# Optimization experiments

Measured on AMD Instinct MI355X. Metric: run time of the kernel, lower is better.

## Reference

```python
import jax, jax.numpy as jnp
import numpy as np
import math

DIM_IN, DIM_OUT, DIM_HID = 128, 128, 512
DEPTH, HEADS, DIM_HEAD, MLP = 6, 8, 64, 2048
INNER = HEADS * DIM_HEAD  # 512


def _inorm(t, eps=1e-5):
    # torch InstanceNorm1d on ((b h), n, d): normalize over last (spatial) dim, biased var, no affine
    m = jnp.mean(t, axis=-1, keepdims=True)
    v = jnp.mean((t - m) ** 2, axis=-1, keepdims=True)
    return (t - m) * jax.lax.rsqrt(v + eps)


def _layernorm(t, g, b, eps=1e-5):
    m = jnp.mean(t, axis=-1, keepdims=True)
    v = jnp.mean((t - m) ** 2, axis=-1, keepdims=True)
    return (t - m) * jax.lax.rsqrt(v + eps) * g + b


def _pos_encoding(n, d):
    pos = jnp.arange(n, dtype=jnp.float32)[:, None]
    div = jnp.exp(jnp.arange(0, d, 2, dtype=jnp.float32) * (-math.log(10000.0) / d))
    pe = jnp.zeros((n, d), dtype=jnp.float32)
    pe = pe.at[:, 0::2].set(jnp.sin(pos * div))
    pe = pe.at[:, 1::2].set(jnp.cos(pos * div))
    return pe


def setup_inputs() -> dict:
    key = jax.random.key(0)
    ks = jax.random.split(key, 16)
    s = 0.02
    return {
        "x": jax.random.normal(ks[0], (4, 64, 4096, 2), jnp.float32),
        "W_emb": jax.random.normal(ks[1], (DIM_IN, DIM_HID), jnp.float32) * s,
        "b_emb": jnp.zeros((DIM_HID,), jnp.float32),
        "ln_g": jnp.ones((DEPTH, DIM_HID), jnp.float32),
        "ln_b": jnp.zeros((DEPTH, DIM_HID), jnp.float32),
        "Wqkv": jax.random.normal(ks[2], (DEPTH, DIM_HID, 3 * INNER), jnp.float32) * s,
        "Wout": jax.random.normal(ks[3], (DEPTH, INNER, DIM_HID), jnp.float32) * s,
        "b_out": jnp.zeros((DEPTH, DIM_HID), jnp.float32),
        "W1": jax.random.normal(ks[4], (DEPTH, DIM_HID, 2 * MLP), jnp.float32) * s,
        "b1": jnp.zeros((DEPTH, 2 * MLP), jnp.float32),
        "W2": jax.random.normal(ks[5], (DEPTH, MLP, DIM_HID), jnp.float32) * s,
        "b2": jnp.zeros((DEPTH, DIM_HID), jnp.float32),
        "Wd": jax.random.normal(ks[6], (DIM_HID, DIM_OUT), jnp.float32) * s,
        "bd": jnp.zeros((DIM_OUT,), jnp.float32),
    }


def reference(x, W_emb, b_emb, ln_g, ln_b, Wqkv, Wout, b_out, W1, b1, W2, b2, Wd, bd):
    b, t, n, c = x.shape
    h = x.transpose(0, 2, 1, 3).reshape(b, n, t * c)        # [b, n, dim_in]
    h = (h @ W_emb + b_emb) * math.sqrt(DIM_HID)
    h = h + _pos_encoding(n, DIM_HID)[None]                 # positional encoding (dropout=0)
    inv_n = 1.0 / n
    for i in range(DEPTH):
        # PreNorm(LinearAttention) + residual
        y = _layernorm(h, ln_g[i], ln_b[i])
        qkv = y @ Wqkv[i]                                   # [b, n, 3*inner]
        q, k, v = jnp.split(qkv, 3, axis=-1)
        sp = lambda z: z.reshape(b, n, HEADS, DIM_HEAD).transpose(0, 2, 1, 3)  # b h n d
        q, k, v = sp(q), sp(k), sp(v)
        k, v = _inorm(k), _inorm(v)                         # galerkin: norm K and V
        dots = jnp.einsum('bhnd,bhne->bhde', k, v)          # k^T v: O(n) attention
        o = jnp.einsum('bhnd,bhde->bhne', q, dots) * inv_n
        o = o.transpose(0, 2, 1, 3).reshape(b, n, INNER)
        h = o @ Wout[i] + b_out[i] + h
        # FeedForward (no PreNorm in galerkin branch) + residual
        f = h @ W1[i] + b1[i]
        f = jax.nn.gelu(f[..., :MLP], approximate=False) * f[..., MLP:]
        h = f @ W2[i] + b2[i] + h
    out = h @ Wd + bd                                       # [b, n, dim_out]
    return out.transpose(0, 2, 1).reshape(b, -1, 1)         # [b, dim_out*n, 1]
```

## Files before the change

### kernel.cpp

```cpp
#include <hip/hip_runtime.h>
#include <hip/hip_bf16.h>
#include <stdint.h>
#include <math.h>


typedef _Float16 f16x8 __attribute__((ext_vector_type(8)));
typedef float f32x4 __attribute__((ext_vector_type(4)));
typedef unsigned short u16x8 __attribute__((ext_vector_type(8)));
typedef unsigned short u16;

#define SEQ 4096
#define NTOK 16384
#define HID 512
#define RSCL 256.0f
#define RSCLI (1.0f/256.0f)

__device__ __forceinline__ float wred(float x) {
#pragma unroll
  for (int off = 32; off; off >>= 1) x += __shfl_xor(x, off);
  return x;
}

__device__ __forceinline__ u16 f2h(float v) {
  _Float16 h = (_Float16)v;
  return __builtin_bit_cast(u16, h);
}
__device__ __forceinline__ float h2f(u16 u) {
  return (float)__builtin_bit_cast(_Float16, u);
}

__device__ __forceinline__ float fgelu(float a) {
  float t = 0.7978845608f * a * (1.0f + 0.044715f * a * a);
  float e = __expf(2.0f * t);
  float th = 1.0f - 2.0f / (e + 1.0f);
  return 0.5f * a * (1.0f + th);
}

__device__ __forceinline__ void gload16(const void* g, void* l) {
  __builtin_amdgcn_global_load_lds(
      reinterpret_cast<const __attribute__((address_space(1))) int*>(
          reinterpret_cast<uintptr_t>(g)),
      reinterpret_cast<__attribute__((address_space(3))) int*>(
          reinterpret_cast<uintptr_t>(l)),
      16, 0, 0);
}

__device__ __forceinline__ void stS(const u16* g, int ldk, int rowBase, int k0,
                                    short* lds, int c) {
  int pr = c >> 3, s8 = (c & 7) ^ (pr & 7);
  int r = pr * 2 + (s8 >> 2);
  gload16(g + (size_t)(rowBase + r) * ldk + k0 + (s8 & 3) * 8, lds + c * 8);
}
__device__ __forceinline__ int idxg(int row, int grp) {
  int pr = row >> 1;
  int s8 = ((((row & 1) << 2) | grp) ^ (pr & 7));
  return pr * 64 + s8 * 8;
}

__global__ __launch_bounds__(256) void k_transpose(const float* __restrict__ src,
                                                   u16* __restrict__ dst,
                                                   int K, int N) {
  int d = blockIdx.z;
  const float* s = src + (size_t)d * K * N;
  u16* o = dst + (size_t)d * N * K;
  int k0 = blockIdx.x * 64, n0 = blockIdx.y * 64;
  __shared__ float tile[64][65];
  int t = threadIdx.x, c = t & 63, r4 = t >> 6;
#pragma unroll
  for (int i = 0; i < 16; ++i) {
    int r = i * 4 + r4;
    tile[r][c] = s[(size_t)(k0 + r) * N + n0 + c];
  }
  __syncthreads();
#pragma unroll
  for (int i = 0; i < 16; ++i) {
    int r = i * 4 + r4;
    o[(size_t)(n0 + r) * K + k0 + c] = f2h(tile[c][r]);
  }
}

__global__ __launch_bounds__(256) void k_packx(const float* __restrict__ x,
                                               u16* __restrict__ XP) {
  int idx = blockIdx.x * 256 + threadIdx.x;
  int k = idx & 127, row = idx >> 7;
  int b = row >> 12, n = row & 4095;
  int tt = k >> 1, c = k & 1;
  XP[idx] = f2h(x[(((size_t)(b * 64 + tt)) * SEQ + n) * 2 + c]);
}

__global__ __launch_bounds__(256) void k_ln(const float* __restrict__ H,
                                            const float* __restrict__ G,
                                            const float* __restrict__ B,
                                            u16* __restrict__ Y) {
  int t = threadIdx.x, lane = t & 63;
  int row = blockIdx.x * 4 + (t >> 6);
  const float4* h4 = (const float4*)(H + (size_t)row * HID);
  float4 a = h4[lane * 2], b = h4[lane * 2 + 1];
  float v[8] = {a.x, a.y, a.z, a.w, b.x, b.y, b.z, b.w};
  float s = v[0] + v[1] + v[2] + v[3] + v[4] + v[5] + v[6] + v[7];
  s = wred(s);
  float m = s * (1.0f / 512.0f);
  float q = 0.f;
#pragma unroll
  for (int i = 0; i < 8; ++i) {
    v[i] -= m;
    q += v[i] * v[i];
  }
  q = wred(q);
  float rs = rsqrtf(q * (1.0f / 512.0f) + 1e-5f);
  const float4* g4 = (const float4*)G;
  const float4* b4 = (const float4*)B;
  float4 g1 = g4[lane * 2], g2 = g4[lane * 2 + 1];
  float4 e1 = b4[lane * 2], e2 = b4[lane * 2 + 1];
  float gg[8] = {g1.x, g1.y, g1.z, g1.w, g2.x, g2.y, g2.z, g2.w};
  float ee[8] = {e1.x, e1.y, e1.z, e1.w, e2.x, e2.y, e2.z, e2.w};
  union { u16x8 v; u16 s_[8]; } uh;
#pragma unroll
  for (int i = 0; i < 8; ++i) uh.s_[i] = f2h(v[i] * rs * gg[i] + ee[i]);
  *reinterpret_cast<u16x8*>((u16*)Y + (size_t)row * HID + lane * 8) = uh.v;
}

__global__ __launch_bounds__(256) void k_dots(const u16* __restrict__ QKV,
                                              float* __restrict__ DOTSP) {
  int bh = blockIdx.y, b = bh >> 3, h = bh & 7;
  int n0 = blockIdx.x * 512;
  __shared__ alignas(16) short ks[64 * 64];
  __shared__ alignas(16) short vs[64 * 64];
  int t = threadIdx.x;
  int d0 = (t & 15) * 4, e0 = (t >> 4) * 4;
  float acc[4][4] = {};
  for (int sub = 0; sub < 8; ++sub) {
    int nb = n0 + sub * 64;
#pragma unroll
    for (int i = 0; i < 2; ++i) {
      int c = t + i * 256;
      int r = c >> 3, off = (c & 7) << 3;
      const u16* base = QKV + (size_t)(b * SEQ + nb + r) * 1536;
      gload16(base + 512 + h * 64 + off, ks + c * 8);
      gload16(base + 1024 + h * 64 + off, vs + c * 8);
    }
    asm volatile("s_waitcnt vmcnt(0)" ::: "memory");
    __syncthreads();
    for (int r = 0; r < 64; ++r) {
      short4 kk = *(const short4*)&ks[r * 64 + d0];
      short4 vv = *(const short4*)&vs[r * 64 + e0];
      float kf[4] = {h2f((u16)kk.x), h2f((u16)kk.y), h2f((u16)kk.z), h2f((u16)kk.w)};
      float vf[4] = {h2f((u16)vv.x), h2f((u16)vv.y), h2f((u16)vv.z), h2f((u16)vv.w)};
#pragma unroll
      for (int i = 0; i < 4; ++i)
#pragma unroll
        for (int j = 0; j < 4; ++j) acc[i][j] += kf[i] * vf[j];
    }
    __syncthreads();
  }
  float* dst = DOTSP + ((size_t)blockIdx.x * 32 + bh) * 4096;
#pragma unroll
  for (int i = 0; i < 4; ++i)
#pragma unroll
    for (int j = 0; j < 4; ++j) dst[(d0 + i) * 64 + e0 + j] = acc[i][j];
}

__global__ __launch_bounds__(256) void k_reddots(const float* __restrict__ P,
                                                 float* __restrict__ D) {
  int i = blockIdx.x * 256 + threadIdx.x;
  float s = 0.f;
#pragma unroll
  for (int c = 0; c < 8; ++c) s += P[(size_t)c * 131072 + i];
  D[i] = s;
}

__global__ __launch_bounds__(256) void k_ov(const u16* __restrict__ QKV,
                                            const float* __restrict__ DOTS,
                                            u16* __restrict__ O) {
  int bh = blockIdx.y, b = bh >> 3, h = bh & 7;
  int n0 = blockIdx.x * 64;
  __shared__ alignas(16) float ds[64 * 64];
  __shared__ alignas(16) short qs[64 * 64];
  int t = threadIdx.x;
  const float* dsrc = DOTS + (size_t)bh * 4096;
#pragma unroll
  for (int i = 0; i < 16; ++i) ds[t + i * 256] = dsrc[t + i * 256];
#pragma unroll
  for (int i = 0; i < 2; ++i) {
    int c = t + i * 256, r = c >> 3, off = (c & 7) << 3;
    gload16(QKV + (size_t)(b * SEQ + n0 + r) * 1536 + h * 64 + off, qs + c * 8);
  }
  asm volatile("s_waitcnt vmcnt(0)" ::: "memory");
  __syncthreads();
  int wv = t >> 6, lane = t & 63;
  for (int tok = wv; tok < 64; tok += 4) {
    float acc = 0.f;
#pragma unroll
    for (int d = 0; d < 64; d += 4) {
      short4 q4 = *(const short4*)&qs[tok * 64 + d];
      acc += h2f((u16)q4.x) * ds[(d + 0) * 64 + lane];
      acc += h2f((u16)q4.y) * ds[(d + 1) * 64 + lane];
      acc += h2f((u16)q4.z) * ds[(d + 2) * 64 + lane];
      acc += h2f((u16)q4.w) * ds[(d + 3) * 64 + lane];
    }
    O[(size_t)(b * SEQ + n0 + tok) * 512 + h * 64 + lane] = f2h(acc * (1.0f / SEQ));
  }
}

template <int MODE>
__global__ __launch_bounds__(256, 2) void k_gemm(
    const u16* __restrict__ A, const u16* __restrict__ B1, int K,
    const float* __restrict__ bias, const float* __restrict__ Hin,
    float ascale, float* __restrict__ out32, u16* __restrict__ o16, int ldo) {
  __shared__ alignas(16) short sm[2][2][4096];
  const int t = threadIdx.x, lane = t & 63;
  const int wv = t >> 6, wr = wv >> 1, wc = wv & 1;
  const int r16 = lane & 15, grp = lane >> 4;
  const int mBase = blockIdx.y * 128, nBase = blockIdx.x * 128;
  const int NT = K >> 5;

  f32x4 acc[4][4] = {};

  auto stage_all = [&](int sb, int k0) {
    stS(A, K, mBase, k0, &sm[sb][0][0], t);
    stS(A, K, mBase, k0, &sm[sb][0][0], t + 256);
    stS(B1, K, nBase, k0, &sm[sb][1][0], t);
    stS(B1, K, nBase, k0, &sm[sb][1][0], t + 256);
  };

  stage_all(0, 0);
  stage_all(1, 32);

  for (int kt = 0; kt < NT; ++kt) {
    const int cur = kt & 1;
    if (kt + 1 < NT) asm volatile("s_waitcnt vmcnt(4)" ::: "memory");
    else             asm volatile("s_waitcnt vmcnt(0)" ::: "memory");
    __builtin_amdgcn_s_barrier();
    f16x8 af[4], bv[4];
#pragma unroll
    for (int f = 0; f < 4; ++f)
      af[f] = *(const f16x8*)&sm[cur][0][idxg(wr * 64 + f * 16 + r16, grp)];
#pragma unroll
    for (int f = 0; f < 4; ++f)
      bv[f] = *(const f16x8*)&sm[cur][1][idxg(wc * 64 + f * 16 + r16, grp)];
    asm volatile("s_waitcnt lgkmcnt(0)" ::: "memory");
    __builtin_amdgcn_sched_barrier(0);
    __builtin_amdgcn_s_barrier();
    if (kt + 2 < NT) stage_all(cur, (kt + 2) << 5);
    __builtin_amdgcn_s_setprio(1);
#pragma unroll
    for (int i = 0; i < 4; ++i)
#pragma unroll
      for (int j = 0; j < 4; ++j)
        acc[i][j] = __builtin_amdgcn_mfma_f32_16x16x32_f16(af[i], bv[j], acc[i][j], 0, 0, 0);
    __builtin_amdgcn_s_setprio(0);
  }

  if constexpr (MODE == 1) {
    const bool doNorm = (nBase >= 512);
#pragma unroll
    for (int i = 0; i < 4; ++i) {
#pragma unroll
      for (int r = 0; r < 4; ++r) {
        float s = 0.f, s2 = 0.f;
#pragma unroll
        for (int j = 0; j < 4; ++j) {
          float v = acc[i][j][r];
          s += v;
          s2 += v * v;
        }
#pragma unroll
        for (int off = 8; off; off >>= 1) {
          s += __shfl_xor(s, off);
          s2 += __shfl_xor(s2, off);
        }
        float m = s * (1.0f / 64.0f);
        float var = fmaxf(s2 * (1.0f / 64.0f) - m * m, 0.f);
        float rs = rsqrtf(var + 1e-5f);
        int row = mBase + wr * 64 + i * 16 + grp * 4 + r;
#pragma unroll
        for (int j = 0; j < 4; ++j) {
          int col = nBase + wc * 64 + j * 16 + r16;
          float v = acc[i][j][r];
          if (doNorm) v = (v - m) * rs;
          o16[(size_t)row * ldo + col] = f2h(v);
        }
      }
    }
    return;
  }

#pragma unroll
  for (int i = 0; i < 4; ++i) {
#pragma unroll
    for (int j = 0; j < 4; ++j) {
#pragma unroll
      for (int r = 0; r < 4; ++r) {
        int row = mBase + wr * 64 + i * 16 + grp * 4 + r;
        int col = nBase + wc * 64 + j * 16 + r16;
        float v = acc[i][j][r];
        if constexpr (MODE == 0) {
          v = (v + bias[col]) * 22.627416997969522f;
          int n = row & (SEQ - 1);
          int k2 = col >> 1;
          float ang = (float)n * expf((float)k2 * -0.03597789207803197f);
          v += (col & 1) ? cosf(ang) : sinf(ang);
          out32[(size_t)row * HID + col] = v;
        } else if constexpr (MODE == 2) {
          v = v * ascale + bias[col] + Hin[(size_t)row * HID + col];
          out32[(size_t)row * HID + col] = v;
          o16[(size_t)row * HID + col] = f2h(v * RSCLI);
        } else {
          v = v * RSCL + bias[col];
          out32[(size_t)(row >> 12) * (128 * 4096) + (size_t)col * SEQ + (row & 4095)] = v;
        }
      }
    }
  }
}

__global__ __launch_bounds__(512, 2) void k_gemmG(
    const u16* __restrict__ A, int lda,
    const u16* __restrict__ B1, const u16* __restrict__ B2, int K,
    const float* __restrict__ bias, u16* __restrict__ o16, int ldo) {
  __shared__ alignas(16) short sm[2][20480];
  const int t = threadIdx.x, lane = t & 63;
  const int w = t >> 6, wr = w >> 2, wcn = w & 3;
  const int r16 = lane & 15, grp = lane >> 4;
  const int mBase = blockIdx.y * 128, nBase = blockIdx.x * 256;
  const int NT = K >> 5;

  f32x4 acc[4][4] = {};
  f32x4 acc2[4][4] = {};

  auto stage_all = [&](int sb, int k0) {
    stS(A, lda, mBase, k0, &sm[sb][0], t);
    stS(B1, K, nBase, k0, &sm[sb][4096], t);
    stS(B1, K, nBase, k0, &sm[sb][4096], t + 512);
    stS(B2, K, nBase, k0, &sm[sb][12288], t);
    stS(B2, K, nBase, k0, &sm[sb][12288], t + 512);
  };

  stage_all(0, 0);
  stage_all(1, 32);

  for (int kt = 0; kt < NT; ++kt) {
    const int cur = kt & 1;
    if (kt + 1 < NT) asm volatile("s_waitcnt vmcnt(5)" ::: "memory");
    else             asm volatile("s_waitcnt vmcnt(0)" ::: "memory");
    __builtin_amdgcn_s_barrier();
    f16x8 af[4], b1v[4], b2v[4];
#pragma unroll
    for (int i = 0; i < 4; ++i)
      af[i] = *(const f16x8*)&sm[cur][idxg(wr * 64 + i * 16 + r16, grp)];
#pragma unroll
    for (int j = 0; j < 4; ++j) {
      int ro = idxg(wcn * 64 + j * 16 + r16, grp);
      b1v[j] = *(const f16x8*)&sm[cur][4096 + ro];
      b2v[j] = *(const f16x8*)&sm[cur][12288 + ro];
    }
    asm volatile("s_waitcnt lgkmcnt(0)" ::: "memory");
    __builtin_amdgcn_sched_barrier(0);
    __builtin_amdgcn_s_barrier();
    if (kt + 2 < NT) stage_all(cur, (kt + 2) << 5);
    __builtin_amdgcn_s_setprio(1);
#pragma unroll
    for (int i = 0; i < 4; ++i)
#pragma unroll
      for (int j = 0; j < 4; ++j) {
        acc[i][j] = __builtin_amdgcn_mfma_f32_16x16x32_f16(af[i], b1v[j], acc[i][j], 0, 0, 0);
        acc2[i][j] = __builtin_amdgcn_mfma_f32_16x16x32_f16(af[i], b2v[j], acc2[i][j], 0, 0, 0);
      }
    __builtin_amdgcn_s_setprio(0);
  }

#pragma unroll
  for (int i = 0; i < 4; ++i) {
#pragma unroll
    for (int j = 0; j < 4; ++j) {
#pragma unroll
      for (int r = 0; r < 4; ++r) {
        int row = mBase + wr * 64 + i * 16 + grp * 4 + r;
        int col = nBase + wcn * 64 + j * 16 + r16;
        float a = acc[i][j][r] * RSCL + bias[col];
        float c2 = acc2[i][j][r] * RSCL + bias[2048 + col];
        o16[(size_t)row * ldo + col] = f2h(fgelu(a) * c2 * RSCLI);
      }
    }
  }
}

extern "C" void kernel_launch(void* const* d_in, const int* in_sizes, int n_in,
                              void* d_out, int out_size, void* d_ws, size_t ws_size,
                              hipStream_t stream) {
  const float* x    = (const float*)d_in[0];
  const float* Wemb = (const float*)d_in[1];
  const float* bemb = (const float*)d_in[2];
  const float* lng  = (const float*)d_in[3];
  const float* lnb  = (const float*)d_in[4];
  const float* Wqkv = (const float*)d_in[5];
  const float* Wout = (const float*)d_in[6];
  const float* bout = (const float*)d_in[7];
  const float* W1   = (const float*)d_in[8];
  const float* b1   = (const float*)d_in[9];
  const float* W2   = (const float*)d_in[10];
  const float* b2   = (const float*)d_in[11];
  const float* Wd   = (const float*)d_in[12];
  const float* bd   = (const float*)d_in[13];

  char* p = (char*)d_ws;
  auto alloc = [&](size_t bytes) {
    char* r = p;
    p += (bytes + 255) & ~(size_t)255;
    return r;
  };
  u16* WembT = (u16*)alloc((size_t)512 * 128 * 2);
  u16* WqkvT = (u16*)alloc((size_t)6 * 1536 * 512 * 2);
  u16* WoutT = (u16*)alloc((size_t)6 * 512 * 512 * 2);
  u16* W1T   = (u16*)alloc((size_t)6 * 4096 * 512 * 2);
  u16* W2T   = (u16*)alloc((size_t)6 * 512 * 2048 * 2);
  u16* WdT   = (u16*)alloc((size_t)128 * 512 * 2);
  float* H   = (float*)alloc((size_t)NTOK * 512 * 4);
  u16* HB    = (u16*)alloc((size_t)NTOK * 512 * 2);
  float* DOTSP = (float*)alloc((size_t)8 * 32 * 4096 * 4);
  float* DOTS  = (float*)alloc((size_t)32 * 4096 * 4);
  char* U = alloc((size_t)64 * 1024 * 1024);
  const size_t MI = 1024 * 1024;
  u16* XP  = (u16*)U;
  u16* Y   = (u16*)U;
  u16* QKV = (u16*)(U + 16 * MI);
  u16* O   = (u16*)U;
  u16* F   = (u16*)U;

  k_transpose<<<dim3(2, 8, 1),  256, 0, stream>>>(Wemb, WembT, 128, 512);
  k_transpose<<<dim3(8, 24, 6), 256, 0, stream>>>(Wqkv, WqkvT, 512, 1536);
  k_transpose<<<dim3(8, 8, 6),  256, 0, stream>>>(Wout, WoutT, 512, 512);
  k_transpose<<<dim3(8, 64, 6), 256, 0, stream>>>(W1, W1T, 512, 4096);
  k_transpose<<<dim3(32, 8, 6), 256, 0, stream>>>(W2, W2T, 2048, 512);
  k_transpose<<<dim3(8, 2, 1),  256, 0, stream>>>(Wd, WdT, 512, 128);

  k_packx<<<8192, 256, 0, stream>>>(x, XP);
  k_gemm<0><<<dim3(4, 128), 256, 0, stream>>>(XP, WembT, 128, bemb,
      nullptr, 1.f, H, nullptr, 0);

  for (int i = 0; i < 6; ++i) {
    k_ln<<<4096, 256, 0, stream>>>(H, lng + i * 512, lnb + i * 512, Y);
    k_gemm<1><<<dim3(12, 128), 256, 0, stream>>>(Y,
        WqkvT + (size_t)i * 1536 * 512, 512, nullptr, nullptr, 1.f,
        nullptr, QKV, 1536);
    k_dots<<<dim3(8, 32), 256, 0, stream>>>(QKV, DOTSP);
    k_reddots<<<512, 256, 0, stream>>>(DOTSP, DOTS);
    k_ov<<<dim3(64, 32), 256, 0, stream>>>(QKV, DOTS, O);
    k_gemm<2><<<dim3(4, 128), 256, 0, stream>>>(O,
        WoutT + (size_t)i * 512 * 512, 512, bout + i * 512, H, 1.f, H, HB, 512);
    k_gemmG<<<dim3(8, 128), 512, 0, stream>>>(HB, 512,
        W1T + (size_t)i * 4096 * 512,
        W1T + (size_t)i * 4096 * 512 + (size_t)2048 * 512, 512,
        b1 + i * 4096, F, 2048);
    k_gemm<2><<<dim3(4, 128), 256, 0, stream>>>(F,
        W2T + (size_t)i * 512 * 2048, 2048, b2 + i * 512, H, RSCL, H, HB, 512);
  }
  k_gemm<7><<<dim3(1, 128), 256, 0, stream>>>(HB, WdT, 512, bd,
      nullptr, 1.f, (float*)d_out, nullptr, 0);
}
```

Measured before the change: 1.815 ms.

## Stage K/V/Q as fp32 in LDS, register-tile o=q·dots, move GEMM restaging after MFMAs

k_dots and k_ov now load fp16 QKV through registers, convert to fp32 once and store fp32 tiles in LDS, so the inner loops no longer convert halves repeatedly. k_ov switches from one token per wave with scalar LDS reads to a 4x4 register tile per thread with float4 loads and vectorized stores. Both GEMM kernels move the barrier and next-stage global-to-LDS load to after the MFMA block, so fragment reads no longer wait on an extra barrier. The cost is double the LDS footprint for the staging tiles and less overlap between the next tile's loads and the MFMAs.

```diff
diff --git a/kernel.cpp b/kernel.cpp
--- a/kernel.cpp
+++ b/kernel.cpp
@@ -124,34 +124,47 @@
                                               float* __restrict__ DOTSP) {
   int bh = blockIdx.y, b = bh >> 3, h = bh & 7;
   int n0 = blockIdx.x * 512;
-  __shared__ alignas(16) short ks[64 * 64];
-  __shared__ alignas(16) short vs[64 * 64];
+  __shared__ alignas(16) float ksf[64 * 64];
+  __shared__ alignas(16) float vsf[64 * 64];
   int t = threadIdx.x;
   int d0 = (t & 15) * 4, e0 = (t >> 4) * 4;
   float acc[4][4] = {};
   for (int sub = 0; sub < 8; ++sub) {
     int nb = n0 + sub * 64;
+    u16x8 kreg[2], vreg[2];
+    int rr[2], oo[2];
 #pragma unroll
     for (int i = 0; i < 2; ++i) {
       int c = t + i * 256;
-      int r = c >> 3, off = (c & 7) << 3;
-      const u16* base = QKV + (size_t)(b * SEQ + nb + r) * 1536;
-      gload16(base + 512 + h * 64 + off, ks + c * 8);
-      gload16(base + 1024 + h * 64 + off, vs + c * 8);
-    }
-    asm volatile("s_waitcnt vmcnt(0)" ::: "memory");
+      rr[i] = c >> 3;
+      oo[i] = (c & 7) << 3;
+      const u16* base = QKV + (size_t)(b * SEQ + nb + rr[i]) * 1536 + h * 64 + oo[i];
+      kreg[i] = *(const u16x8*)(base + 512);
+      vreg[i] = *(const u16x8*)(base + 1024);
+    }
+    __syncthreads();
+#pragma unroll
+    for (int i = 0; i < 2; ++i) {
+      float4 k0 = {h2f(kreg[i][0]), h2f(kreg[i][1]), h2f(kreg[i][2]), h2f(kreg[i][3])};
+      float4 k1 = {h2f(kreg[i][4]), h2f(kreg[i][5]), h2f(kreg[i][6]), h2f(kreg[i][7])};
+      float4 v0 = {h2f(vreg[i][0]), h2f(vreg[i][1]), h2f(vreg[i][2]), h2f(vreg[i][3])};
+      float4 v1 = {h2f(vreg[i][4]), h2f(vreg[i][5]), h2f(vreg[i][6]), h2f(vreg[i][7])};
+      *(float4*)&ksf[rr[i] * 64 + oo[i]] = k0;
+      *(float4*)&ksf[rr[i] * 64 + oo[i] + 4] = k1;
+      *(float4*)&vsf[rr[i] * 64 + oo[i]] = v0;
+      *(float4*)&vsf[rr[i] * 64 + oo[i] + 4] = v1;
+    }
     __syncthreads();
     for (int r = 0; r < 64; ++r) {
-      short4 kk = *(const short4*)&ks[r * 64 + d0];
-      short4 vv = *(const short4*)&vs[r * 64 + e0];
-      float kf[4] = {h2f((u16)kk.x), h2f((u16)kk.y), h2f((u16)kk.z), h2f((u16)kk.w)};
-      float vf[4] = {h2f((u16)vv.x), h2f((u16)vv.y), h2f((u16)vv.z), h2f((u16)vv.w)};
+      float4 kk = *(const float4*)&ksf[r * 64 + d0];
+      float4 vv = *(const float4*)&vsf[r * 64 + e0];
+      float kf[4] = {kk.x, kk.y, kk.z, kk.w};
+      float vf[4] = {vv.x, vv.y, vv.z, vv.w};
 #pragma unroll
       for (int i = 0; i < 4; ++i)
 #pragma unroll
         for (int j = 0; j < 4; ++j) acc[i][j] += kf[i] * vf[j];
     }
-    __syncthreads();
   }
   float* dst = DOTSP + ((size_t)blockIdx.x * 32 + bh) * 4096;
 #pragma unroll
@@ -175,30 +188,55 @@
   int bh = blockIdx.y, b = bh >> 3, h = bh & 7;
   int n0 = blockIdx.x * 64;
   __shared__ alignas(16) float ds[64 * 64];
-  __shared__ alignas(16) short qs[64 * 64];
+  __shared__ alignas(16) float qsf[64 * 64];
   int t = threadIdx.x;
   const float* dsrc = DOTS + (size_t)bh * 4096;
 #pragma unroll
-  for (int i = 0; i < 16; ++i) ds[t + i * 256] = dsrc[t + i * 256];
+  for (int i = 0; i < 4; ++i) {
+    int c = t + i * 256;
+    *(float4*)&ds[c * 4] = *(const float4*)&dsrc[c * 4];
+  }
+  u16x8 qreg[2];
+  int qr[2], qo[2];
 #pragma unroll
   for (int i = 0; i < 2; ++i) {
-    int c = t + i * 256, r = c >> 3, off = (c & 7) << 3;
-    gload16(QKV + (size_t)(b * SEQ + n0 + r) * 1536 + h * 64 + off, qs + c * 8);
-  }
-  asm volatile("s_waitcnt vmcnt(0)" ::: "memory");
+    int c = t + i * 256;
+    qr[i] = c >> 3;
+    qo[i] = (c & 7) << 3;
+    qreg[i] = *(const u16x8*)(QKV + (size_t)(b * SEQ + n0 + qr[i]) * 1536 + h * 64 + qo[i]);
+  }
+#pragma unroll
+  for (int i = 0; i < 2; ++i) {
+    float4 q0 = {h2f(qreg[i][0]), h2f(qreg[i][1]), h2f(qreg[i][2]), h2f(qreg[i][3])};
+    float4 q1 = {h2f(qreg[i][4]), h2f(qreg[i][5]), h2f(qreg[i][6]), h2f(qreg[i][7])};
+    *(float4*)&qsf[qr[i] * 64 + qo[i]] = q0;
+    *(float4*)&qsf[qr[i] * 64 + qo[i] + 4] = q1;
+  }
   __syncthreads();
-  int wv = t >> 6, lane = t & 63;
-  for (int tok = wv; tok < 64; tok += 4) {
-    float acc = 0.f;
-#pragma unroll
-    for (int d = 0; d < 64; d += 4) {
-      short4 q4 = *(const short4*)&qs[tok * 64 + d];
-      acc += h2f((u16)q4.x) * ds[(d + 0) * 64 + lane];
-      acc += h2f((u16)q4.y) * ds[(d + 1) * 64 + lane];
-      acc += h2f((u16)q4.z) * ds[(d + 2) * 64 + lane];
-      acc += h2f((u16)q4.w) * ds[(d + 3) * 64 + lane];
-    }
-    O[(size_t)(b * SEQ + n0 + tok) * 512 + h * 64 + lane] = f2h(acc * (1.0f / SEQ));
+  int t0 = (t & 15) * 4, e0 = (t >> 4) * 4;
+  float acc[4][4] = {};
+  for (int dq = 0; dq < 16; ++dq) {
+    float4 d0v = *(const float4*)&ds[(dq * 4 + 0) * 64 + e0];
+    float4 d1v = *(const float4*)&ds[(dq * 4 + 1) * 64 + e0];
+    float4 d2v = *(const float4*)&ds[(dq * 4 + 2) * 64 + e0];
+    float4 d3v = *(const float4*)&ds[(dq * 4 + 3) * 64 + e0];
+#pragma unroll
+    for (int i = 0; i < 4; ++i) {
+      float4 qv = *(const float4*)&qsf[(t0 + i) * 64 + dq * 4];
+      acc[i][0] += qv.x * d0v.x + qv.y * d1v.x + qv.z * d2v.x + qv.w * d3v.x;
+      acc[i][1] += qv.x * d0v.y + qv.y * d1v.y + qv.z * d2v.y + qv.w * d3v.y;
+      acc[i][2] += qv.x * d0v.z + qv.y * d1v.z + qv.z * d2v.z + qv.w * d3v.z;
+      acc[i][3] += qv.x * d0v.w + qv.y * d1v.w + qv.z * d2v.w + qv.w * d3v.w;
+    }
+  }
+#pragma unroll
+  for (int i = 0; i < 4; ++i) {
+    short4 o4;
+    o4.x = (short)f2h(acc[i][0] * (1.0f / SEQ));
+    o4.y = (short)f2h(acc[i][1] * (1.0f / SEQ));
+    o4.z = (short)f2h(acc[i][2] * (1.0f / SEQ));
+    o4.w = (short)f2h(acc[i][3] * (1.0f / SEQ));
+    *(short4*)((u16*)O + (size_t)(b * SEQ + n0 + t0 + i) * 512 + h * 64 + e0) = o4;
   }
 }
 
@@ -238,10 +276,6 @@
 #pragma unroll
     for (int f = 0; f < 4; ++f)
       bv[f] = *(const f16x8*)&sm[cur][1][idxg(wc * 64 + f * 16 + r16, grp)];
-    asm volatile("s_waitcnt lgkmcnt(0)" ::: "memory");
-    __builtin_amdgcn_sched_barrier(0);
-    __builtin_amdgcn_s_barrier();
-    if (kt + 2 < NT) stage_all(cur, (kt + 2) << 5);
     __builtin_amdgcn_s_setprio(1);
 #pragma unroll
     for (int i = 0; i < 4; ++i)
@@ -249,6 +283,9 @@
       for (int j = 0; j < 4; ++j)
         acc[i][j] = __builtin_amdgcn_mfma_f32_16x16x32_f16(af[i], bv[j], acc[i][j], 0, 0, 0);
     __builtin_amdgcn_s_setprio(0);
+    asm volatile("s_waitcnt lgkmcnt(0)" ::: "memory");
+    __builtin_amdgcn_s_barrier();
+    if (kt + 2 < NT) stage_all(cur, (kt + 2) << 5);
   }
 
   if constexpr (MODE == 1) {
@@ -354,10 +391,6 @@
       b1v[j] = *(const f16x8*)&sm[cur][4096 + ro];
       b2v[j] = *(const f16x8*)&sm[cur][12288 + ro];
     }
-    asm volatile("s_waitcnt lgkmcnt(0)" ::: "memory");
-    __builtin_amdgcn_sched_barrier(0);
-    __builtin_amdgcn_s_barrier();
-    if (kt + 2 < NT) stage_all(cur, (kt + 2) << 5);
     __builtin_amdgcn_s_setprio(1);
 #pragma unroll
     for (int i = 0; i < 4; ++i)
@@ -367,6 +400,9 @@
         acc2[i][j] = __builtin_amdgcn_mfma_f32_16x16x32_f16(af[i], b2v[j], acc2[i][j], 0, 0, 0);
       }
     __builtin_amdgcn_s_setprio(0);
+    asm volatile("s_waitcnt lgkmcnt(0)" ::: "memory");
+    __builtin_amdgcn_s_barrier();
+    if (kt + 2 < NT) stage_all(cur, (kt + 2) << 5);
   }
 
 #pragma unroll
```

Result: slower. 1.991 ms (+9.7%).
